# Optimization experiments

Hardware: AMD Instinct MI355X
Metric: run time of the kernel (lower is better)

The kernel has to match this reference:

```python
import jax, jax.numpy as jnp
import numpy as np

D, H, L, MLP = 1024, 16, 4, 4096
DH = D // H
EPS = 1e-5
SCALE_BASE = 512.0  # rotary_embedding_torch xpos default

def _ln(x, w, b):
    m = jnp.mean(x, axis=-1, keepdims=True)
    v = jnp.mean((x - m) ** 2, axis=-1, keepdims=True)
    return (x - m) * jax.lax.rsqrt(v + EPS) * w + b

def _rotate_half(x):
    # interleaved pair rotation: (x0, x1) -> (-x1, x0)
    x1, x2 = x[..., 0::2], x[..., 1::2]
    return jnp.stack((-x2, x1), axis=-1).reshape(x.shape)

def _rope_tables(S):
    inv = 1.0 / (10000.0 ** (jnp.arange(0, DH, 2, dtype=jnp.float32) / DH))
    pos = jnp.arange(S, dtype=jnp.float32)
    freqs = jnp.repeat(pos[:, None] * inv[None, :], 2, axis=-1)      # [S, DH]
    base = (jnp.arange(0, DH, 2, dtype=jnp.float32) + 0.4 * DH) / (1.4 * DH)
    power = (pos - S // 2) / SCALE_BASE
    scale = jnp.repeat(base[None, :] ** power[:, None], 2, axis=-1)  # [S, DH] xpos scale
    return jnp.cos(freqs), jnp.sin(freqs), scale

def setup_inputs() -> dict:
    key = jax.random.key(0)
    ks = jax.random.split(key, 8)
    B, S = 4, 1024
    w = 0.02
    return {
        "x": jax.random.normal(ks[0], (B, S, D), jnp.float32),
        "ln1_w": jnp.ones((L, D), jnp.float32), "ln1_b": jnp.zeros((L, D), jnp.float32),
        "wqkv": jax.random.normal(ks[1], (L, D, 3 * D), jnp.float32) * w,
        "bqkv": jnp.zeros((L, 3 * D), jnp.float32),
        "wo": jax.random.normal(ks[2], (L, D, D), jnp.float32) * w,
        "bo": jnp.zeros((L, D), jnp.float32),
        "ln2_w": jnp.ones((L, D), jnp.float32), "ln2_b": jnp.zeros((L, D), jnp.float32),
        "w1": jax.random.normal(ks[3], (L, D, MLP), jnp.float32) * w,
        "b1": jnp.zeros((L, MLP), jnp.float32),
        "w2": jax.random.normal(ks[4], (L, D, MLP), jnp.float32) * w,
        "b2": jnp.zeros((L, MLP), jnp.float32),
        "wout": jax.random.normal(ks[5], (L, MLP, D), jnp.float32) * w,
        "bout": jnp.zeros((L, D), jnp.float32),
        "fln_w": jnp.ones((D,), jnp.float32), "fln_b": jnp.zeros((D,), jnp.float32),
    }

def reference(x, ln1_w, ln1_b, wqkv, bqkv, wo, bo, ln2_w, ln2_b,
              w1, b1, w2, b2, wout, bout, fln_w, fln_b):
    B, S, _ = x.shape
    cos, sin, scale = _rope_tables(S)
    cos, sin, scale = cos[:, None, :], sin[:, None, :], scale[:, None, :]  # [S,1,DH] bcast heads
    inv_scale = 1.0 / scale
    attn_scale = DH ** -0.5
    for l in range(L):
        normed = _ln(x, ln1_w[l], ln1_b[l])
        qkv = (normed @ wqkv[l] + bqkv[l]).reshape(B, S, 3, H, DH)
        q, k, v = qkv[:, :, 0], qkv[:, :, 1], qkv[:, :, 2]  # [B,S,H,DH]
        q = (q * cos + _rotate_half(q) * sin) * scale       # xpos rotary, queries
        k = (k * cos + _rotate_half(k) * sin) * inv_scale   # xpos rotary, keys (scale**-1)
        attn = jnp.einsum('bihd,bjhd->bhij', q, k) * attn_scale
        attn = jax.nn.softmax(attn, axis=-1)
        y = jnp.einsum('bhij,bjhd->bihd', attn, v).reshape(B, S, D)
        x = x + y @ wo[l] + bo[l]
        h = _ln(x, ln2_w[l], ln2_b[l])
        ff = (jax.nn.silu(h @ w1[l] + b1[l]) * (h @ w2[l] + b2[l])) @ wout[l] + bout[l]
        x = x + ff
    return _ln(x, fln_w, fln_b)
```

## Files before the change

### kernel.cpp

```cpp
#include <hip/hip_runtime.h>
#include <hip/hip_bf16.h>
#include <math.h>


#define TD 1024
#define TH 16
#define TDH 64
#define TL 4
#define TMLP 4096
#define TB 4
#define TS 1024
#define TM (TB*TS)

typedef __attribute__((ext_vector_type(8))) short short8;
typedef __attribute__((ext_vector_type(4))) float f32x4;
typedef __attribute__((ext_vector_type(4))) unsigned short us4;
typedef __attribute__((ext_vector_type(2))) unsigned short us2;

__device__ __forceinline__ float bf2f(unsigned short u) {
  union { unsigned int i; float f; } x; x.i = ((unsigned int)u) << 16; return x.f;
}
__device__ __forceinline__ unsigned short f2bf(float f) {
  unsigned int x = __float_as_uint(f);
  unsigned int r = (x + 0x7FFFu + ((x >> 16) & 1u)) >> 16;
  return (unsigned short)r;
}

#if defined(__has_builtin)
#if __has_builtin(__builtin_amdgcn_global_load_lds)
#define TE_HAS_GLL 1
#endif
#endif

__device__ __forceinline__ void stage16(void* lds, const void* g) {
#ifdef TE_HAS_GLL
  __builtin_amdgcn_global_load_lds(
      (const __attribute__((address_space(1))) void*)g,
      (__attribute__((address_space(3))) void*)lds, 16, 0, 0);
#else
  *(short8*)lds = *(const short8*)g;
#endif
}

#define MFMA_BF16(a,b,c) __builtin_amdgcn_mfma_f32_16x16x32_bf16((a),(b),(c),0,0,0)

__global__ __launch_bounds__(256)
void te_tab(float4* __restrict__ tab) {
  int idx = blockIdx.x * 256 + threadIdx.x;
  int s = idx >> 5, i = idx & 31;
  float inv = powf(10000.0f, -(2.0f * (float)i) / 64.0f);
  float fr = (float)s * inv;
  float c = cosf(fr), sn = sinf(fr);
  float base = (2.0f * (float)i + 0.4f * 64.0f) / (1.4f * 64.0f);
  float p = ((float)s - 512.0f) / 512.0f;
  float scl = powf(base, p);
  float4 t;
  t.x = c; t.y = sn; t.z = scl * 0.125f; t.w = 1.0f / scl;
  tab[idx] = t;
}

__global__ __launch_bounds__(256)
void te_transpose_cvt(const float* __restrict__ src, unsigned short* __restrict__ dst,
                      int K, int N) {
  __shared__ float tile[32][33];
  int n0 = blockIdx.x * 32, k0 = blockIdx.y * 32;
  int tx = threadIdx.x, ty = threadIdx.y;
  #pragma unroll
  for (int j = 0; j < 4; ++j)
    tile[ty + 8*j][tx] = src[(size_t)(k0 + ty + 8*j) * N + n0 + tx];
  __syncthreads();
  #pragma unroll
  for (int j = 0; j < 4; ++j)
    dst[(size_t)(n0 + ty + 8*j) * K + k0 + tx] = f2bf(tile[tx][ty + 8*j]);
}

template<int OUTBF>
__global__ __launch_bounds__(256)
void te_ln(const float* __restrict__ in, const float* __restrict__ w,
           const float* __restrict__ b, void* __restrict__ outp) {
  int row = blockIdx.x, t = threadIdx.x;
  float4 v = ((const float4*)(in + (size_t)row * TD))[t];
  float s = v.x + v.y + v.z + v.w;
  float sq = v.x*v.x + v.y*v.y + v.z*v.z + v.w*v.w;
  #pragma unroll
  for (int o = 1; o < 64; o <<= 1) { s += __shfl_xor(s, o); sq += __shfl_xor(sq, o); }
  __shared__ float red[8];
  int wv = t >> 6;
  if ((t & 63) == 0) { red[wv] = s; red[4 + wv] = sq; }
  __syncthreads();
  s  = red[0] + red[1] + red[2] + red[3];
  sq = red[4] + red[5] + red[6] + red[7];
  float mean = s * (1.0f / TD);
  float rstd = rsqrtf(sq * (1.0f / TD) - mean * mean + 1e-5f);
  float4 w4 = ((const float4*)w)[t];
  float4 b4 = ((const float4*)b)[t];
  float r0 = (v.x - mean) * rstd * w4.x + b4.x;
  float r1 = (v.y - mean) * rstd * w4.y + b4.y;
  float r2 = (v.z - mean) * rstd * w4.z + b4.z;
  float r3 = (v.w - mean) * rstd * w4.w + b4.w;
  if (OUTBF) {
    us4 pk; pk[0] = f2bf(r0); pk[1] = f2bf(r1); pk[2] = f2bf(r2); pk[3] = f2bf(r3);
    ((us4*)outp)[(size_t)row * (TD/4) + t] = pk;
  } else {
    float4 o; o.x = r0; o.y = r1; o.z = r2; o.w = r3;
    ((float4*)outp)[(size_t)row * (TD/4) + t] = o;
  }
}

template<int MODE>
__global__ __launch_bounds__(256)
void te_gemm(const unsigned short* __restrict__ A, const unsigned short* __restrict__ Bt,
             const float* __restrict__ bias, const float* resid,
             const unsigned short* __restrict__ gate, void* outp,
             int M, int N, int K) {
  __shared__ short As[128 * 32];
  __shared__ short Bs[128 * 32];
  int bm = blockIdx.x, bn = blockIdx.y;
  int t = threadIdx.x;
  int lane = t & 63, w = t >> 6;
  int wr = w >> 1, wc = w & 1;
  int lr = lane & 15, lk = lane >> 4;
  f32x4 acc[4][4] = {};

  int srow = t >> 2, scol = (t & 3) * 8;
  const short* Ap = (const short*)A + (size_t)(bm * 128 + srow) * K + scol;
  const short* Bp = (const short*)Bt + (size_t)(bn * 128 + srow) * K + scol;
  short* Al = As + t * 8;
  short* Bl = Bs + t * 8;
  const size_t stride64 = (size_t)64 * K;
  int nk = K >> 5;
  for (int kt = 0; kt < nk; ++kt) {
    __syncthreads();
    stage16(Al,        Ap);
    stage16(Al + 2048, Ap + stride64);
    stage16(Bl,        Bp);
    stage16(Bl + 2048, Bp + stride64);
    Ap += 32; Bp += 32;
    __syncthreads();
    short8 af[4], bfv[4];
    #pragma unroll
    for (int mi = 0; mi < 4; ++mi)
      af[mi] = *(const short8*)&As[(wr*64 + mi*16 + lr) * 32 + lk*8];
    #pragma unroll
    for (int nj = 0; nj < 4; ++nj)
      bfv[nj] = *(const short8*)&Bs[(wc*64 + nj*16 + lr) * 32 + lk*8];
    #pragma unroll
    for (int mi = 0; mi < 4; ++mi)
      #pragma unroll
      for (int nj = 0; nj < 4; ++nj)
        acc[mi][nj] = MFMA_BF16(af[mi], bfv[nj], acc[mi][nj]);
  }
  #pragma unroll
  for (int mi = 0; mi < 4; ++mi) {
    #pragma unroll
    for (int nj = 0; nj < 4; ++nj) {
      int col = bn*128 + wc*64 + nj*16 + lr;
      float bv = bias[col];
      #pragma unroll
      for (int r = 0; r < 4; ++r) {
        int row = bm*128 + wr*64 + mi*16 + lk*4 + r;
        size_t o = (size_t)row * N + col;
        float val = acc[mi][nj][r] + bv;
        if (MODE == 0) {
          ((unsigned short*)outp)[o] = f2bf(val);
        } else if (MODE == 1) {
          ((float*)outp)[o] = resid[o] + val;
        } else {
          float a = bf2f(gate[o]);
          float sg = a / (1.0f + __expf(-a));
          ((unsigned short*)outp)[o] = f2bf(sg * val);
        }
      }
    }
  }
}

__global__ __launch_bounds__(256)
void te_rope(const unsigned short* __restrict__ qkv, const float4* __restrict__ tab,
             unsigned short* __restrict__ qb, unsigned short* __restrict__ kb) {
  int idx = blockIdx.x * 256 + threadIdx.x;
  int i = idx & 31;
  int h = (idx >> 5) & 15;
  int row = idx >> 9;
  int s = row & (TS - 1);
  float4 t4 = tab[(s << 5) + i];
  size_t base = (size_t)row * (3*TD) + h * TDH + 2*i;
  us2 qp = *(const us2*)&qkv[base];
  us2 kp = *(const us2*)&qkv[base + TD];
  float qe = bf2f(qp[0]), qo = bf2f(qp[1]);
  float ke = bf2f(kp[0]), ko = bf2f(kp[1]);
  size_t ob = (size_t)row * TD + h * TDH + 2*i;
  us2 qo2, ko2;
  qo2[0] = f2bf((qe * t4.x - qo * t4.y) * t4.z);
  qo2[1] = f2bf((qo * t4.x + qe * t4.y) * t4.z);
  ko2[0] = f2bf((ke * t4.x - ko * t4.y) * t4.w);
  ko2[1] = f2bf((ko * t4.x + ke * t4.y) * t4.w);
  *(us2*)&qb[ob] = qo2;
  *(us2*)&kb[ob] = ko2;
}

__global__ __launch_bounds__(256)
void te_attn(const unsigned short* __restrict__ qb, const unsigned short* __restrict__ kb,
             const unsigned short* __restrict__ qkv, unsigned short* __restrict__ y) {
  __shared__ char Ks[8192];
  __shared__ char Vs[8192];
  __shared__ char Ps[4][2048];
  int qt = blockIdx.x;
  int bh = blockIdx.y;
  int b = bh >> 4, h = bh & 15;
  int t = threadIdx.x, lane = t & 63, w = t >> 6;
  int lq = lane & 15, lg = lane >> 4;

  const unsigned short* vptr = qkv + 2*TD;

  int qrow = b*TS + qt*64 + w*16 + lq;
  short8 aq0 = *(const short8*)&qb[(size_t)qrow*TD + h*TDH + lg*8];
  short8 aq1 = *(const short8*)&qb[(size_t)qrow*TD + h*TDH + 32 + lg*8];

  f32x4 oacc[4] = {};
  float rm[4] = {-3e38f, -3e38f, -3e38f, -3e38f};
  float rl[4] = {0.f, 0.f, 0.f, 0.f};

  int srr = t >> 3;
  int scb = (t & 7) * 8;

  for (int kt = 0; kt < TS/64; ++kt) {
    int kbase = b*TS + kt*64;
    __syncthreads();
    #pragma unroll
    for (int half = 0; half < 2; ++half) {
      int row = srr + half*32;
      short8 d = *(const short8*)&kb[(size_t)(kbase + row)*TD + h*TDH + scb];
      int off = (row*128 + scb*2) ^ ((row & 7) << 4);
      *(short8*)&Ks[off] = d;
    }
    #pragma unroll
    for (int half = 0; half < 2; ++half) {
      int dh = srr + half*32;
      short8 d;
      #pragma unroll
      for (int i = 0; i < 8; ++i)
        d[i] = (short)vptr[(size_t)(kbase + scb + i)*(3*TD) + h*TDH + dh];
      int off = (dh*128 + scb*2) ^ ((dh & 7) << 4);
      *(short8*)&Vs[off] = d;
    }
    __syncthreads();
    f32x4 sc[4];
    #pragma unroll
    for (int nj = 0; nj < 4; ++nj) {
      int row = nj*16 + lq;
      int sw = (row & 7) << 4;
      short8 b0 = *(const short8*)&Ks[(row*128 + lg*16) ^ sw];
      short8 b1 = *(const short8*)&Ks[(row*128 + 64 + lg*16) ^ sw];
      f32x4 c = {};
      c = MFMA_BF16(aq0, b0, c);
      c = MFMA_BF16(aq1, b1, c);
      sc[nj] = c;
    }
    float mn[4], al[4];
    #pragma unroll
    for (int r = 0; r < 4; ++r) {
      float x = fmaxf(fmaxf(sc[0][r], sc[1][r]), fmaxf(sc[2][r], sc[3][r]));
      #pragma unroll
      for (int o = 1; o < 16; o <<= 1) x = fmaxf(x, __shfl_xor(x, o));
      mn[r] = fmaxf(rm[r], x);
      al[r] = __expf(rm[r] - mn[r]);
      rm[r] = mn[r];
    }
    #pragma unroll
    for (int nj = 0; nj < 4; ++nj)
      #pragma unroll
      for (int r = 0; r < 4; ++r)
        sc[nj][r] = __expf(sc[nj][r] - mn[r]);
    #pragma unroll
    for (int r = 0; r < 4; ++r) {
      float x = sc[0][r] + sc[1][r] + sc[2][r] + sc[3][r];
      #pragma unroll
      for (int o = 1; o < 16; o <<= 1) x += __shfl_xor(x, o);
      rl[r] = rl[r] * al[r] + x;
    }
    #pragma unroll
    for (int d0 = 0; d0 < 4; ++d0)
      #pragma unroll
      for (int r = 0; r < 4; ++r)
        oacc[d0][r] *= al[r];
    #pragma unroll
    for (int nj = 0; nj < 4; ++nj)
      #pragma unroll
      for (int r = 0; r < 4; ++r) {
        int row = lg*4 + r;
        int off = (row*128 + (nj*16 + lq)*2) ^ ((row & 7) << 4);
        *(short*)&Ps[w][off] = (short)f2bf(sc[nj][r]);
      }
    short8 pa0, pa1;
    {
      int sw = (lq & 7) << 4;
      pa0 = *(const short8*)&Ps[w][(lq*128 + lg*16) ^ sw];
      pa1 = *(const short8*)&Ps[w][(lq*128 + 64 + lg*16) ^ sw];
    }
    #pragma unroll
    for (int d0 = 0; d0 < 4; ++d0) {
      int row = d0*16 + lq;
      int sw = (row & 7) << 4;
      short8 b0 = *(const short8*)&Vs[(row*128 + lg*16) ^ sw];
      short8 b1 = *(const short8*)&Vs[(row*128 + 64 + lg*16) ^ sw];
      oacc[d0] = MFMA_BF16(pa0, b0, oacc[d0]);
      oacc[d0] = MFMA_BF16(pa1, b1, oacc[d0]);
    }
  }
  #pragma unroll
  for (int d0 = 0; d0 < 4; ++d0)
    #pragma unroll
    for (int r = 0; r < 4; ++r) {
      int row = b*TS + qt*64 + w*16 + lg*4 + r;
      float val = oacc[d0][r] / rl[r];
      y[(size_t)row*TD + h*TDH + d0*16 + lq] = f2bf(val);
    }
}

extern "C" void kernel_launch(void* const* d_in, const int* in_sizes, int n_in,
                              void* d_out, int out_size, void* d_ws, size_t ws_size,
                              hipStream_t stream) {
  const float* x_in = (const float*)d_in[0];
  const float* ln1w = (const float*)d_in[1];
  const float* ln1b = (const float*)d_in[2];
  const float* wqkv = (const float*)d_in[3];
  const float* bqkv = (const float*)d_in[4];
  const float* wo   = (const float*)d_in[5];
  const float* bo   = (const float*)d_in[6];
  const float* ln2w = (const float*)d_in[7];
  const float* ln2b = (const float*)d_in[8];
  const float* w1   = (const float*)d_in[9];
  const float* b1   = (const float*)d_in[10];
  const float* w2   = (const float*)d_in[11];
  const float* b2   = (const float*)d_in[12];
  const float* wout = (const float*)d_in[13];
  const float* bout = (const float*)d_in[14];
  const float* flnw = (const float*)d_in[15];
  const float* flnb = (const float*)d_in[16];

  char* ws = (char*)d_ws;
  size_t off = 0;
  auto alloc = [&](size_t bytes) -> void* {
    void* p = ws + off;
    off += (bytes + 255) & ~(size_t)255;
    return p;
  };
  unsigned short* wqkv_t = (unsigned short*)alloc((size_t)3*TD*TD*2);
  unsigned short* wo_t   = (unsigned short*)alloc((size_t)TD*TD*2);
  unsigned short* w1_t   = (unsigned short*)alloc((size_t)TMLP*TD*2);
  unsigned short* w2_t   = (unsigned short*)alloc((size_t)TMLP*TD*2);
  unsigned short* wout_t = (unsigned short*)alloc((size_t)TD*TMLP*2);
  float*          x      = (float*)alloc((size_t)TM*TD*4);
  unsigned short* nrm    = (unsigned short*)alloc((size_t)TM*TD*2);
  unsigned short* u1     = (unsigned short*)alloc((size_t)TM*TMLP*2);
  unsigned short* qbuf   = (unsigned short*)alloc((size_t)TM*TD*2);
  unsigned short* kbuf   = (unsigned short*)alloc((size_t)TM*TD*2);
  unsigned short* u2     = (unsigned short*)alloc((size_t)TM*TMLP*2);
  float4*         tab    = (float4*)alloc((size_t)TS*32*sizeof(float4));

  dim3 blk256(256);
  dim3 tblk(32, 8);
  te_tab<<<dim3(TS*32/256), blk256, 0, stream>>>(tab);
  hipMemcpyAsync(x, x_in, (size_t)TM*TD*4, hipMemcpyDeviceToDevice, stream);

  for (int l = 0; l < TL; ++l) {
    te_transpose_cvt<<<dim3(3*TD/32, TD/32), tblk, 0, stream>>>(
        wqkv + (size_t)l*TD*3*TD, wqkv_t, TD, 3*TD);
    te_transpose_cvt<<<dim3(TD/32, TD/32), tblk, 0, stream>>>(
        wo + (size_t)l*TD*TD, wo_t, TD, TD);
    te_transpose_cvt<<<dim3(TMLP/32, TD/32), tblk, 0, stream>>>(
        w1 + (size_t)l*TD*TMLP, w1_t, TD, TMLP);
    te_transpose_cvt<<<dim3(TMLP/32, TD/32), tblk, 0, stream>>>(
        w2 + (size_t)l*TD*TMLP, w2_t, TD, TMLP);
    te_transpose_cvt<<<dim3(TD/32, TMLP/32), tblk, 0, stream>>>(
        wout + (size_t)l*TMLP*TD, wout_t, TMLP, TD);

    te_ln<1><<<dim3(TM), blk256, 0, stream>>>(x, ln1w + l*TD, ln1b + l*TD, nrm);
    te_gemm<0><<<dim3(TM/128, 3*TD/128), blk256, 0, stream>>>(
        nrm, wqkv_t, bqkv + l*3*TD, nullptr, nullptr, u1, TM, 3*TD, TD);
    te_rope<<<dim3(TM*TH*32/256), blk256, 0, stream>>>(u1, tab, qbuf, kbuf);
    te_attn<<<dim3(TS/64, TB*TH), blk256, 0, stream>>>(qbuf, kbuf, u1, u2);
    te_gemm<1><<<dim3(TM/128, TD/128), blk256, 0, stream>>>(
        u2, wo_t, bo + l*TD, x, nullptr, x, TM, TD, TD);
    te_ln<1><<<dim3(TM), blk256, 0, stream>>>(x, ln2w + l*TD, ln2b + l*TD, nrm);
    te_gemm<0><<<dim3(TM/128, TMLP/128), blk256, 0, stream>>>(
        nrm, w1_t, b1 + l*TMLP, nullptr, nullptr, u1, TM, TMLP, TD);
    te_gemm<2><<<dim3(TM/128, TMLP/128), blk256, 0, stream>>>(
        nrm, w2_t, b2 + l*TMLP, nullptr, u1, u2, TM, TMLP, TD);
    te_gemm<1><<<dim3(TM/128, TD/128), blk256, 0, stream>>>(
        u2, wout_t, bout + l*TD, x, nullptr, x, TM, TD, TMLP);
  }
  te_ln<0><<<dim3(TM), blk256, 0, stream>>>(x, flnw, flnb, (float*)d_out);

  (void)in_sizes; (void)n_in; (void)out_size; (void)ws_size;
}
```

Baseline: 1.928 ms.

## Double-buffer GEMM LDS tiles with BK=64 and XOR-swizzled layout

```diff
diff --git a/kernel.cpp b/kernel.cpp
--- a/kernel.cpp
+++ b/kernel.cpp
@@ -113,8 +113,8 @@
              const float* __restrict__ bias, const float* resid,
              const unsigned short* __restrict__ gate, void* outp,
              int M, int N, int K) {
-  __shared__ short As[128 * 32];
-  __shared__ short Bs[128 * 32];
+  __shared__ short As[2][128 * 64];
+  __shared__ short Bs[2][128 * 64];
   int bm = blockIdx.x, bn = blockIdx.y;
   int t = threadIdx.x;
   int lane = t & 63, w = t >> 6;
@@ -122,34 +122,60 @@
   int lr = lane & 15, lk = lane >> 4;
   f32x4 acc[4][4] = {};
 
-  int srow = t >> 2, scol = (t & 3) * 8;
-  const short* Ap = (const short*)A + (size_t)(bm * 128 + srow) * K + scol;
-  const short* Bp = (const short*)Bt + (size_t)(bn * 128 + srow) * K + scol;
-  short* Al = As + t * 8;
-  short* Bl = Bs + t * 8;
-  const size_t stride64 = (size_t)64 * K;
-  int nk = K >> 5;
+  const short* Abase = (const short*)A + (size_t)(bm * 128) * K;
+  const short* Bbase = (const short*)Bt + (size_t)(bn * 128) * K;
+  int srow[4], scol[4];
+  #pragma unroll
+  for (int j = 0; j < 4; ++j) {
+    int m = j * 256 + t;
+    int r = m >> 3, c = m & 7;
+    srow[j] = r;
+    scol[j] = (c ^ (r & 7)) * 8;
+  }
+
+  auto stage_tile = [&](int buf, int k0) {
+    #pragma unroll
+    for (int j = 0; j < 4; ++j) {
+      stage16(&As[buf][j * 2048 + t * 8], Abase + (size_t)srow[j] * K + k0 + scol[j]);
+      stage16(&Bs[buf][j * 2048 + t * 8], Bbase + (size_t)srow[j] * K + k0 + scol[j]);
+    }
+  };
+
+  auto compute_tile = [&](int buf) {
+    #pragma unroll
+    for (int ks = 0; ks < 2; ++ks) {
+      short8 af[4], bfv[4];
+      #pragma unroll
+      for (int mi = 0; mi < 4; ++mi) {
+        int row = wr * 64 + mi * 16 + lr;
+        int cc = (ks * 4 + lk) ^ (row & 7);
+        af[mi] = *(const short8*)&As[buf][row * 64 + cc * 8];
+      }
+      #pragma unroll
+      for (int nj = 0; nj < 4; ++nj) {
+        int row = wc * 64 + nj * 16 + lr;
+        int cc = (ks * 4 + lk) ^ (row & 7);
+        bfv[nj] = *(const short8*)&Bs[buf][row * 64 + cc * 8];
+      }
+      #pragma unroll
+      for (int mi = 0; mi < 4; ++mi)
+        #pragma unroll
+        for (int nj = 0; nj < 4; ++nj)
+          acc[mi][nj] = MFMA_BF16(af[mi], bfv[nj], acc[mi][nj]);
+    }
+  };
+
+  int nk = K >> 6;
+  stage_tile(0, 0);
+  __syncthreads();
+  int cur = 0;
   for (int kt = 0; kt < nk; ++kt) {
+    if (kt + 1 < nk) stage_tile(cur ^ 1, (kt + 1) << 6);
+    compute_tile(cur);
     __syncthreads();
-    stage16(Al,        Ap);
-    stage16(Al + 2048, Ap + stride64);
-    stage16(Bl,        Bp);
-    stage16(Bl + 2048, Bp + stride64);
-    Ap += 32; Bp += 32;
-    __syncthreads();
-    short8 af[4], bfv[4];
-    #pragma unroll
-    for (int mi = 0; mi < 4; ++mi)
-      af[mi] = *(const short8*)&As[(wr*64 + mi*16 + lr) * 32 + lk*8];
-    #pragma unroll
-    for (int nj = 0; nj < 4; ++nj)
-      bfv[nj] = *(const short8*)&Bs[(wc*64 + nj*16 + lr) * 32 + lk*8];
-    #pragma unroll
-    for (int mi = 0; mi < 4; ++mi)
-      #pragma unroll
-      for (int nj = 0; nj < 4; ++nj)
-        acc[mi][nj] = MFMA_BF16(af[mi], bfv[nj], acc[mi][nj]);
-  }
+    cur ^= 1;
+  }
+
   #pragma unroll
   for (int mi = 0; mi < 4; ++mi) {
     #pragma unroll
```

Measured after the change: 1.726 ms. -10.5%, faster.
